# Kernel optimization log

Measured on AMD Instinct MI355X. Metric: run time of the kernel, lower is better.

Reference implementation:

```python
import jax, jax.numpy as jnp
import numpy as np

N_NODES = 50000
N_EDGES = 800000
N_GRAPHS = 128
IN_F = 768
NHID = 64
HID2 = NHID * 2  # 128
N_CLS = 2


def setup_inputs() -> dict:
    key = jax.random.key(0)
    ks = jax.random.split(key, 16)
    s = lambda k, shp, fan: jax.random.normal(k, shp, jnp.float32) / np.sqrt(fan)
    return {
        "x": jax.random.normal(ks[0], (N_NODES, IN_F), jnp.float32),
        "edge_index": jax.random.randint(ks[1], (2, N_EDGES), 0, N_NODES, jnp.int64),
        "batch": jnp.sort(jax.random.randint(ks[2], (N_NODES,), 0, N_GRAPHS, jnp.int64)),
        "W1": s(ks[3], (IN_F, HID2), IN_F),
        "as1": s(ks[4], (HID2,), HID2),
        "ad1": s(ks[5], (HID2,), HID2),
        "b1": jnp.zeros((HID2,), jnp.float32),
        "W2": s(ks[6], (HID2, HID2), HID2),
        "as2": s(ks[7], (HID2,), HID2),
        "ad2": s(ks[8], (HID2,), HID2),
        "b2": jnp.zeros((HID2,), jnp.float32),
        "fc1_w": s(ks[9], (HID2, NHID), HID2),
        "fc1_b": jnp.zeros((NHID,), jnp.float32),
        "fc2_w": s(ks[10], (NHID, N_CLS), NHID),
        "fc2_b": jnp.zeros((N_CLS,), jnp.float32),
    }


def _gat_conv(x, W, a_src, a_dst, b, src, dst):
    # PyG GATConv, heads=1, self-loops already included in (src, dst).
    xw = x @ W                                   # [N, F_out]
    e_src = xw @ a_src                           # [N]
    e_dst = xw @ a_dst                           # [N]
    e = jax.nn.leaky_relu(e_src[src] + e_dst[dst], 0.2)   # [E]
    m = jax.ops.segment_max(e, dst, num_segments=N_NODES)  # per-dst max (stable softmax)
    num = jnp.exp(e - m[dst])
    den = jax.ops.segment_sum(num, dst, num_segments=N_NODES)
    alpha = num / den[dst]                       # [E]
    out = jax.ops.segment_sum(alpha[:, None] * xw[src], dst, num_segments=N_NODES)
    return out + b


def reference(x, edge_index, batch, W1, as1, ad1, b1, W2, as2, ad2, b2,
              fc1_w, fc1_b, fc2_w, fc2_b):
    # add self loops (PyG GATConv default add_self_loops=True)
    loops = jnp.arange(N_NODES, dtype=edge_index.dtype)
    src = jnp.concatenate([edge_index[0], loops])
    dst = jnp.concatenate([edge_index[1], loops])

    h = jax.nn.selu(_gat_conv(x, W1, as1, ad1, b1, src, dst))
    h = jax.nn.selu(_gat_conv(h, W2, as2, ad2, b2, src, dst))

    # global mean pool over graphs
    sums = jax.ops.segment_sum(h, batch, num_segments=N_GRAPHS)          # [G, HID2]
    cnts = jax.ops.segment_sum(jnp.ones((N_NODES,), h.dtype), batch, num_segments=N_GRAPHS)
    pooled = jax.nn.selu(sums / jnp.maximum(cnts, 1.0)[:, None])

    g = jax.nn.selu(pooled @ fc1_w + fc1_b)      # dropout is identity in eval mode
    logits = g @ fc2_w + fc2_b
    return jax.nn.log_softmax(logits, axis=-1)
```

## Files before the change

kernel.cpp:

```cpp
#include <hip/hip_runtime.h>
#include <math.h>

#define N_NODES  50000
#define N_EDGES  800000
#define E_TOT    (N_EDGES + N_NODES)
#define N_GRAPHS 128
#define IN_F     768
#define HID2     128
#define NHID     64

typedef __attribute__((ext_vector_type(8))) short bf16x8;
typedef __attribute__((ext_vector_type(4))) float f32x4;
typedef __attribute__((ext_vector_type(4))) unsigned short us4;

__device__ __forceinline__ float selu_f(float x) {
    const float alpha = 1.6732632423543772f;
    const float scale = 1.0507009873554805f;
    return scale * (x > 0.f ? x : alpha * (expf(x) - 1.f));
}

__device__ __forceinline__ unsigned short f2bf(float f) {
    unsigned u = __float_as_uint(f);
    u += 0x7FFFu + ((u >> 16) & 1u);
    return (unsigned short)(u >> 16);
}
__device__ __forceinline__ float bflo(unsigned q) { return __uint_as_float(q << 16); }
__device__ __forceinline__ float bfhi(unsigned q) { return __uint_as_float(q & 0xffff0000u); }

__global__ void setup_k(const float* __restrict__ W1, const float* __restrict__ W2,
                        unsigned short* __restrict__ Wt1, unsigned short* __restrict__ Wt2,
                        unsigned* __restrict__ deg,
                        float* __restrict__ es1, float* __restrict__ ed1,
                        float* __restrict__ es2, float* __restrict__ ed2) {
    int i = blockIdx.x * blockDim.x + threadIdx.x;
    if (i < N_NODES) {
        deg[i] = 0u;
        es1[i] = 0.f; ed1[i] = 0.f;
        es2[i] = 0.f; ed2[i] = 0.f;
    }
    if (i < 128 * IN_F) {
        int n = i / IN_F, k = i - n * IN_F;
        Wt1[i] = f2bf(W1[(long)k * 128 + n]);
    }
    if (i < 128 * HID2) {
        int n = i >> 7, k = i & 127;
        Wt2[i] = f2bf(W2[(long)k * 128 + n]);
    }
}

#define LDA2 72
template<bool ABF16, bool OUTBF16>
__global__ __launch_bounds__(256) void gemm_mfma(
        const void* __restrict__ Av, const unsigned short* __restrict__ Bt,
        void* __restrict__ Cv, int M, int K,
        const float* __restrict__ a_s, const float* __restrict__ a_d,
        float* __restrict__ es, float* __restrict__ ed) {
    __shared__ unsigned short As[64 * LDA2];
    __shared__ unsigned short Bs[128 * LDA2];
    const float* Af = (const float*)Av;
    const unsigned short* Ab = (const unsigned short*)Av;
    const int tid  = threadIdx.x;
    const int row0 = blockIdx.x * 64;
    const int w    = tid >> 6;
    const int lane = tid & 63;
    const int quad = lane >> 4;
    const int l16  = lane & 15;
    const int m_off = (w & 1) * 32;
    const int n_off = (w >> 1) * 64;

    f32x4 acc[2][4];
#pragma unroll
    for (int mi = 0; mi < 2; mi++)
#pragma unroll
        for (int ni = 0; ni < 4; ni++)
            acc[mi][ni] = (f32x4){0.f, 0.f, 0.f, 0.f};

    float4 aR[4];
    bf16x8 aRb[2];
    bf16x8 bR[4];
    if (ABF16) {
#pragma unroll
        for (int i = 0; i < 2; i++) {
            int p = tid + i * 256;
            int r = p >> 3, c8 = p & 7;
            int gr = row0 + r;
            aRb[i] = (gr < M) ? *(const bf16x8*)&Ab[(long)gr * K + c8 * 8]
                              : (bf16x8){0,0,0,0,0,0,0,0};
        }
    } else {
#pragma unroll
        for (int i = 0; i < 4; i++) {
            int p = tid + i * 256;
            int r = p >> 4, c4 = p & 15;
            int gr = row0 + r;
            aR[i] = (gr < M) ? *(const float4*)&Af[(long)gr * K + c4 * 4]
                             : make_float4(0.f, 0.f, 0.f, 0.f);
        }
    }
#pragma unroll
    for (int i = 0; i < 4; i++) {
        int c = tid + i * 256;
        int n = c >> 3, koff = (c & 7) * 8;
        bR[i] = *(const bf16x8*)&Bt[(long)n * K + koff];
    }

    for (int k0 = 0; k0 < K; k0 += 64) {
        if (ABF16) {
#pragma unroll
            for (int i = 0; i < 2; i++) {
                int p = tid + i * 256;
                int r = p >> 3, c8 = p & 7;
                *(bf16x8*)&As[r * LDA2 + c8 * 8] = aRb[i];
            }
        } else {
#pragma unroll
            for (int i = 0; i < 4; i++) {
                int p = tid + i * 256;
                int r = p >> 4, c4 = p & 15;
                us4 o;
                o.x = f2bf(aR[i].x); o.y = f2bf(aR[i].y);
                o.z = f2bf(aR[i].z); o.w = f2bf(aR[i].w);
                *(us4*)&As[r * LDA2 + c4 * 4] = o;
            }
        }
#pragma unroll
        for (int i = 0; i < 4; i++) {
            int c = tid + i * 256;
            int n = c >> 3, koff = (c & 7) * 8;
            *(bf16x8*)&Bs[n * LDA2 + koff] = bR[i];
        }
        __syncthreads();

        if (k0 + 64 < K) {
            int k1 = k0 + 64;
            if (ABF16) {
#pragma unroll
                for (int i = 0; i < 2; i++) {
                    int p = tid + i * 256;
                    int r = p >> 3, c8 = p & 7;
                    int gr = row0 + r;
                    aRb[i] = (gr < M) ? *(const bf16x8*)&Ab[(long)gr * K + k1 + c8 * 8]
                                      : (bf16x8){0,0,0,0,0,0,0,0};
                }
            } else {
#pragma unroll
                for (int i = 0; i < 4; i++) {
                    int p = tid + i * 256;
                    int r = p >> 4, c4 = p & 15;
                    int gr = row0 + r;
                    aR[i] = (gr < M) ? *(const float4*)&Af[(long)gr * K + k1 + c4 * 4]
                                     : make_float4(0.f, 0.f, 0.f, 0.f);
                }
            }
#pragma unroll
            for (int i = 0; i < 4; i++) {
                int c = tid + i * 256;
                int n = c >> 3, koff = (c & 7) * 8;
                bR[i] = *(const bf16x8*)&Bt[(long)n * K + k1 + koff];
            }
        }

        bf16x8 af[2][2], bfr[2][4];
#pragma unroll
        for (int kk = 0; kk < 2; kk++) {
#pragma unroll
            for (int mi = 0; mi < 2; mi++)
                af[kk][mi] = *(const bf16x8*)&As[(m_off + mi * 16 + l16) * LDA2 + kk * 32 + quad * 8];
#pragma unroll
            for (int ni = 0; ni < 4; ni++)
                bfr[kk][ni] = *(const bf16x8*)&Bs[(n_off + ni * 16 + l16) * LDA2 + kk * 32 + quad * 8];
        }
#pragma unroll
        for (int kk = 0; kk < 2; kk++)
#pragma unroll
            for (int mi = 0; mi < 2; mi++)
#pragma unroll
                for (int ni = 0; ni < 4; ni++)
                    acc[mi][ni] = __builtin_amdgcn_mfma_f32_16x16x32_bf16(
                        af[kk][mi], bfr[kk][ni], acc[mi][ni], 0, 0, 0);
        __syncthreads();
    }

    float as_v[4], ad_v[4];
#pragma unroll
    for (int ni = 0; ni < 4; ni++) {
        int col = n_off + ni * 16 + l16;
        as_v[ni] = a_s[col];
        ad_v[ni] = a_d[col];
    }

#pragma unroll
    for (int mi = 0; mi < 2; mi++)
#pragma unroll
        for (int r = 0; r < 4; r++) {
            int row = row0 + m_off + mi * 16 + quad * 4 + r;
            float ps = 0.f, pd = 0.f;
#pragma unroll
            for (int ni = 0; ni < 4; ni++) {
                float v = acc[mi][ni][r];
                ps = fmaf(v, as_v[ni], ps);
                pd = fmaf(v, ad_v[ni], pd);
            }
#pragma unroll
            for (int o = 1; o < 16; o <<= 1) {
                ps += __shfl_xor(ps, o);
                pd += __shfl_xor(pd, o);
            }
            if (row < M) {
                if (l16 == 0) {
                    atomicAdd(es + row, ps);
                    atomicAdd(ed + row, pd);
                }
                if (OUTBF16) {
                    unsigned short* C16 = (unsigned short*)Cv;
#pragma unroll
                    for (int ni = 0; ni < 4; ni++)
                        C16[(long)row * 128 + n_off + ni * 16 + l16] = f2bf(acc[mi][ni][r]);
                } else {
                    float* Cf = (float*)Cv;
#pragma unroll
                    for (int ni = 0; ni < 4; ni++)
                        Cf[(long)row * 128 + n_off + ni * 16 + l16] = acc[mi][ni][r];
                }
            }
        }
}

__global__ void deg_hist(const int* __restrict__ ei, unsigned* __restrict__ deg) {
    int e = blockIdx.x * blockDim.x + threadIdx.x;
    if (e < N_EDGES) atomicAdd(&deg[ei[N_EDGES + e]], 1u);
}

__global__ __launch_bounds__(256) void scan_seed(const unsigned* __restrict__ deg,
                                                 unsigned* __restrict__ row_ptr,
                                                 unsigned* __restrict__ cursor,
                                                 unsigned* __restrict__ csr_src) {
    __shared__ unsigned psum_s[4];
    __shared__ unsigned wsum[4];
    int tid = threadIdx.x;
    int wid = tid >> 6, lane = tid & 63;
    int chunk0 = blockIdx.x * 256;

    unsigned psum = 0;
    for (int i = tid; i < chunk0; i += 256) psum += deg[i] + 1u;
    for (int o = 32; o; o >>= 1) psum += __shfl_xor(psum, o);
    if (lane == 0) psum_s[wid] = psum;

    int i = chunk0 + tid;
    unsigned v = (i < N_NODES) ? deg[i] + 1u : 0u;
    unsigned x = v;
    for (int o = 1; o < 64; o <<= 1) {
        unsigned y = __shfl_up(x, o);
        if (lane >= o) x += y;
    }
    if (lane == 63) wsum[wid] = x;
    __syncthreads();
    unsigned base = psum_s[0] + psum_s[1] + psum_s[2] + psum_s[3];
    unsigned wbase = 0;
    for (int k = 0; k < wid; k++) wbase += wsum[k];
    if (i < N_NODES) {
        unsigned rp = base + wbase + x - v;
        row_ptr[i] = rp;
        csr_src[rp] = (unsigned)i;
        cursor[i] = rp + 1;
        if (i == N_NODES - 1) row_ptr[N_NODES] = rp + v;
    }
}

__global__ void csr_scatter(const int* __restrict__ ei,
                            unsigned* __restrict__ cursor, unsigned* __restrict__ csr_src) {
    int e = blockIdx.x * blockDim.x + threadIdx.x;
    if (e >= N_EDGES) return;
    int d = ei[N_EDGES + e];
    unsigned p = atomicAdd(&cursor[d], 1u);
    csr_src[p] = (unsigned)ei[e];
}

template<bool OUTBF16>
__global__ __launch_bounds__(256) void gat_agg(
        const unsigned* __restrict__ row_ptr, const unsigned* __restrict__ csr_src,
        const float* __restrict__ e_src, const float* __restrict__ e_dst,
        const unsigned short* __restrict__ xw, const float* __restrict__ bias,
        void* __restrict__ outv) {
    __shared__ float2 buf[4][64];
    int wv = threadIdx.x >> 6;
    int node = blockIdx.x * 4 + wv;
    if (node >= N_NODES) return;
    int lane = threadIdx.x & 63;
    int half = lane >> 5;
    int fl   = lane & 31;
    unsigned beg = row_ptr[node], end = row_ptr[node + 1];
    int deg = (int)(end - beg);
    float ed = e_dst[node];
    const unsigned short* xwf = xw + fl * 4;

    float ax = 0.f, ay = 0.f, az = 0.f, aw = 0.f, den = 0.f;
    for (int base = 0; base < deg; base += 64) {
        int i = base + lane;
        float num = 0.f;
        unsigned s = 0u;
        if (i < deg) {
            s = csr_src[beg + i];
            float e = e_src[s] + ed;
            e = e > 0.f ? e : 0.2f * e;
            num = __expf(e);
            den += num;
        }
        float2 pk; pk.x = num; pk.y = __uint_as_float(s);
        buf[wv][lane] = pk;

        int cnt = deg - base; if (cnt > 64) cnt = 64;
        int steps = (cnt + 1) >> 1;
        int t = 0;
        for (; t + 4 <= steps; t += 4) {
            float2 p0 = buf[wv][2 * (t + 0) + half];
            float2 p1 = buf[wv][2 * (t + 1) + half];
            float2 p2 = buf[wv][2 * (t + 2) + half];
            float2 p3 = buf[wv][2 * (t + 3) + half];
            uint2 q0 = *(const uint2*)&xwf[(long)__float_as_uint(p0.y) * HID2];
            uint2 q1 = *(const uint2*)&xwf[(long)__float_as_uint(p1.y) * HID2];
            uint2 q2 = *(const uint2*)&xwf[(long)__float_as_uint(p2.y) * HID2];
            uint2 q3 = *(const uint2*)&xwf[(long)__float_as_uint(p3.y) * HID2];
            ax = fmaf(p0.x, bflo(q0.x), ax); ay = fmaf(p0.x, bfhi(q0.x), ay);
            az = fmaf(p0.x, bflo(q0.y), az); aw = fmaf(p0.x, bfhi(q0.y), aw);
            ax = fmaf(p1.x, bflo(q1.x), ax); ay = fmaf(p1.x, bfhi(q1.x), ay);
            az = fmaf(p1.x, bflo(q1.y), az); aw = fmaf(p1.x, bfhi(q1.y), aw);
            ax = fmaf(p2.x, bflo(q2.x), ax); ay = fmaf(p2.x, bfhi(q2.x), ay);
            az = fmaf(p2.x, bflo(q2.y), az); aw = fmaf(p2.x, bfhi(q2.y), aw);
            ax = fmaf(p3.x, bflo(q3.x), ax); ay = fmaf(p3.x, bfhi(q3.x), ay);
            az = fmaf(p3.x, bflo(q3.y), az); aw = fmaf(p3.x, bfhi(q3.y), aw);
        }
        for (; t < steps; t++) {
            float2 p = buf[wv][2 * t + half];
            uint2 q = *(const uint2*)&xwf[(long)__float_as_uint(p.y) * HID2];
            ax = fmaf(p.x, bflo(q.x), ax); ay = fmaf(p.x, bfhi(q.x), ay);
            az = fmaf(p.x, bflo(q.y), az); aw = fmaf(p.x, bfhi(q.y), aw);
        }
    }
    ax += __shfl_xor(ax, 32); ay += __shfl_xor(ay, 32);
    az += __shfl_xor(az, 32); aw += __shfl_xor(aw, 32);
    for (int o = 32; o; o >>= 1) den += __shfl_xor(den, o);
    float inv = 1.f / den;
    float v0 = selu_f(fmaf(ax, inv, bias[fl * 4 + 0]));
    float v1 = selu_f(fmaf(ay, inv, bias[fl * 4 + 1]));
    float v2 = selu_f(fmaf(az, inv, bias[fl * 4 + 2]));
    float v3 = selu_f(fmaf(aw, inv, bias[fl * 4 + 3]));
    if (half == 0) {
        if (OUTBF16) {
            uint2 o;
            o.x = ((unsigned)f2bf(v1) << 16) | (unsigned)f2bf(v0);
            o.y = ((unsigned)f2bf(v3) << 16) | (unsigned)f2bf(v2);
            *(uint2*)((unsigned short*)outv + (long)node * HID2 + fl * 4) = o;
        } else {
            float4 o = make_float4(v0, v1, v2, v3);
            *(float4*)((float*)outv + (long)node * HID2 + fl * 4) = o;
        }
    }
}

__global__ __launch_bounds__(256) void pool_head(
        const float* __restrict__ h, const int* __restrict__ batch,
        const float* __restrict__ fc1w, const float* __restrict__ fc1b,
        const float* __restrict__ fc2w, const float* __restrict__ fc2b,
        float* __restrict__ out) {
    __shared__ float pooled_s[HID2];
    __shared__ float part[HID2];
    __shared__ float g_s[NHID];
    int g = blockIdx.x;
    int lo = 0, hi = N_NODES;
    while (lo < hi) { int mid = (lo + hi) >> 1; if (batch[mid] < g) lo = mid + 1; else hi = mid; }
    int start = lo;
    hi = N_NODES;
    while (lo < hi) { int mid = (lo + hi) >> 1; if (batch[mid] < g + 1) lo = mid + 1; else hi = mid; }
    int end = lo;

    int f = threadIdx.x & 127, half = threadIdx.x >> 7;
    float acc = 0.f;
    for (int n = start + half; n < end; n += 2) acc += h[(long)n * HID2 + f];
    if (half == 0) part[f] = acc;
    __syncthreads();
    if (half == 1) {
        float c = (float)(end - start);
        c = c > 1.f ? c : 1.f;
        pooled_s[f] = selu_f((part[f] + acc) / c);
    }
    __syncthreads();
    int j = threadIdx.x;
    if (j < NHID) {
        float a = fc1b[j];
#pragma unroll
        for (int k = 0; k < HID2; k++) a = fmaf(pooled_s[k], fc1w[k * NHID + j], a);
        g_s[j] = selu_f(a);
    }
    __syncthreads();
    if (j == 0) {
        float l0 = fc2b[0], l1 = fc2b[1];
#pragma unroll
        for (int k = 0; k < NHID; k++) {
            float v = g_s[k];
            l0 = fmaf(v, fc2w[2 * k + 0], l0);
            l1 = fmaf(v, fc2w[2 * k + 1], l1);
        }
        float m = fmaxf(l0, l1);
        float lse = m + logf(expf(l0 - m) + expf(l1 - m));
        out[g * 2 + 0] = l0 - lse;
        out[g * 2 + 1] = l1 - lse;
    }
}

extern "C" void kernel_launch(void* const* d_in, const int* in_sizes, int n_in,
                              void* d_out, int out_size, void* d_ws, size_t ws_size,
                              hipStream_t stream) {
    const float* x     = (const float*)d_in[0];
    const int*   ei    = (const int*)d_in[1];
    const int*   batch = (const int*)d_in[2];
    const float* W1    = (const float*)d_in[3];
    const float* as1   = (const float*)d_in[4];
    const float* ad1   = (const float*)d_in[5];
    const float* b1    = (const float*)d_in[6];
    const float* W2    = (const float*)d_in[7];
    const float* as2   = (const float*)d_in[8];
    const float* ad2   = (const float*)d_in[9];
    const float* b2    = (const float*)d_in[10];
    const float* fc1w  = (const float*)d_in[11];
    const float* fc1b  = (const float*)d_in[12];
    const float* fc2w  = (const float*)d_in[13];
    const float* fc2b  = (const float*)d_in[14];
    float* out = (float*)d_out;

    const long NH = (long)N_NODES * HID2;
    unsigned short* xwb = (unsigned short*)d_ws;
    unsigned short* h1b = xwb + NH;
    float*    B2      = (float*)(h1b + NH);
    float*    es1     = B2 + NH;
    float*    ed1     = es1 + N_NODES;
    float*    es2     = ed1 + N_NODES;
    float*    ed2     = es2 + N_NODES;
    unsigned* deg     = (unsigned*)(ed2 + N_NODES);
    unsigned* cursor  = deg + N_NODES;
    unsigned* row_ptr = cursor + N_NODES;
    unsigned* csr_src = row_ptr + N_NODES + 1;
    unsigned short* Wt1 = (unsigned short*)(csr_src + E_TOT);
    unsigned short* Wt2 = Wt1 + 128 * IN_F;

    const int TB = 256;
    const int gNode = (N_NODES + TB - 1) / TB;
    const int gEdge = (N_EDGES + TB - 1) / TB;
    const int gGemm = (N_NODES + 63) / 64;
    const int gAgg  = (N_NODES + 3) / 4;

    setup_k<<<(128 * IN_F + TB - 1) / TB, TB, 0, stream>>>(W1, W2, Wt1, Wt2, deg,
                                                           es1, ed1, es2, ed2);
    deg_hist<<<gEdge, TB, 0, stream>>>(ei, deg);
    scan_seed<<<gNode, TB, 0, stream>>>(deg, row_ptr, cursor, csr_src);
    csr_scatter<<<gEdge, TB, 0, stream>>>(ei, cursor, csr_src);

    gemm_mfma<false, true><<<gGemm, 256, 0, stream>>>(x, Wt1, xwb, N_NODES, IN_F,
                                                      as1, ad1, es1, ed1);
    gat_agg<true><<<gAgg, 256, 0, stream>>>(row_ptr, csr_src, es1, ed1, xwb, b1, h1b);

    gemm_mfma<true, true><<<gGemm, 256, 0, stream>>>(h1b, Wt2, xwb, N_NODES, HID2,
                                                     as2, ad2, es2, ed2);
    gat_agg<false><<<gAgg, 256, 0, stream>>>(row_ptr, csr_src, es2, ed2, xwb, b2, B2);

    pool_head<<<N_GRAPHS, 256, 0, stream>>>(B2, batch, fc1w, fc1b, fc2w, fc2b, out);
}
```

Measured before the change: 529.0 us.

## Split GAT aggregation into alpha pass and XCD-partitioned feature-slice gather

GEMM output is now written in a column-slab layout: four slabs of 32 bf16 features, each stored contiguously per node. Attention softmax weights are computed once per edge by a separate alpha kernel into a buffer. A gather kernel then maps each of four feature slabs to a pair of XCDs, chosen from the block id, so that each XCD's L2 only caches a quarter of the feature table. This trades an extra kernel and extra alpha writes and reads for better cache locality in the random gather, and it relies on the assumption that blocks are dispatched round-robin across XCDs.

```diff
diff --git a/kernel.cpp b/kernel.cpp
--- a/kernel.cpp
+++ b/kernel.cpp
@@ -49,10 +49,10 @@
 }
 
 #define LDA2 72
-template<bool ABF16, bool OUTBF16>
+template<bool ABF16>
 __global__ __launch_bounds__(256) void gemm_mfma(
         const void* __restrict__ Av, const unsigned short* __restrict__ Bt,
-        void* __restrict__ Cv, int M, int K,
+        unsigned short* __restrict__ Cq, int M, int K,
         const float* __restrict__ a_s, const float* __restrict__ a_d,
         float* __restrict__ es, float* __restrict__ ed) {
     __shared__ unsigned short As[64 * LDA2];
@@ -211,16 +211,11 @@
                     atomicAdd(es + row, ps);
                     atomicAdd(ed + row, pd);
                 }
-                if (OUTBF16) {
-                    unsigned short* C16 = (unsigned short*)Cv;
-#pragma unroll
-                    for (int ni = 0; ni < 4; ni++)
-                        C16[(long)row * 128 + n_off + ni * 16 + l16] = f2bf(acc[mi][ni][r]);
-                } else {
-                    float* Cf = (float*)Cv;
-#pragma unroll
-                    for (int ni = 0; ni < 4; ni++)
-                        Cf[(long)row * 128 + n_off + ni * 16 + l16] = acc[mi][ni][r];
+#pragma unroll
+                for (int ni = 0; ni < 4; ni++) {
+                    int col = n_off + ni * 16 + l16;
+                    Cq[((long)(col >> 5) * N_NODES + row) * 32 + (col & 31)] =
+                        f2bf(acc[mi][ni][r]);
                 }
             }
         }
@@ -276,85 +271,110 @@
     csr_src[p] = (unsigned)ei[e];
 }
 
-template<bool OUTBF16>
-__global__ __launch_bounds__(256) void gat_agg(
+__global__ __launch_bounds__(256) void gat_alpha(
         const unsigned* __restrict__ row_ptr, const unsigned* __restrict__ csr_src,
         const float* __restrict__ e_src, const float* __restrict__ e_dst,
-        const unsigned short* __restrict__ xw, const float* __restrict__ bias,
-        void* __restrict__ outv) {
-    __shared__ float2 buf[4][64];
-    int wv = threadIdx.x >> 6;
-    int node = blockIdx.x * 4 + wv;
+        float* __restrict__ alpha) {
+    int hw = threadIdx.x >> 5;
+    int node = blockIdx.x * 8 + hw;
     if (node >= N_NODES) return;
-    int lane = threadIdx.x & 63;
-    int half = lane >> 5;
-    int fl   = lane & 31;
+    int l = threadIdx.x & 31;
     unsigned beg = row_ptr[node], end = row_ptr[node + 1];
     int deg = (int)(end - beg);
     float ed = e_dst[node];
-    const unsigned short* xwf = xw + fl * 4;
-
-    float ax = 0.f, ay = 0.f, az = 0.f, aw = 0.f, den = 0.f;
-    for (int base = 0; base < deg; base += 64) {
-        int i = base + lane;
+    float den = 0.f;
+
+    if (deg <= 32) {
         float num = 0.f;
-        unsigned s = 0u;
-        if (i < deg) {
-            s = csr_src[beg + i];
+        if (l < deg) {
+            unsigned s = csr_src[beg + l];
             float e = e_src[s] + ed;
             e = e > 0.f ? e : 0.2f * e;
             num = __expf(e);
-            den += num;
-        }
-        float2 pk; pk.x = num; pk.y = __uint_as_float(s);
-        buf[wv][lane] = pk;
-
-        int cnt = deg - base; if (cnt > 64) cnt = 64;
-        int steps = (cnt + 1) >> 1;
-        int t = 0;
-        for (; t + 4 <= steps; t += 4) {
-            float2 p0 = buf[wv][2 * (t + 0) + half];
-            float2 p1 = buf[wv][2 * (t + 1) + half];
-            float2 p2 = buf[wv][2 * (t + 2) + half];
-            float2 p3 = buf[wv][2 * (t + 3) + half];
-            uint2 q0 = *(const uint2*)&xwf[(long)__float_as_uint(p0.y) * HID2];
-            uint2 q1 = *(const uint2*)&xwf[(long)__float_as_uint(p1.y) * HID2];
-            uint2 q2 = *(const uint2*)&xwf[(long)__float_as_uint(p2.y) * HID2];
-            uint2 q3 = *(const uint2*)&xwf[(long)__float_as_uint(p3.y) * HID2];
-            ax = fmaf(p0.x, bflo(q0.x), ax); ay = fmaf(p0.x, bfhi(q0.x), ay);
-            az = fmaf(p0.x, bflo(q0.y), az); aw = fmaf(p0.x, bfhi(q0.y), aw);
-            ax = fmaf(p1.x, bflo(q1.x), ax); ay = fmaf(p1.x, bfhi(q1.x), ay);
-            az = fmaf(p1.x, bflo(q1.y), az); aw = fmaf(p1.x, bfhi(q1.y), aw);
-            ax = fmaf(p2.x, bflo(q2.x), ax); ay = fmaf(p2.x, bfhi(q2.x), ay);
-            az = fmaf(p2.x, bflo(q2.y), az); aw = fmaf(p2.x, bfhi(q2.y), aw);
-            ax = fmaf(p3.x, bflo(q3.x), ax); ay = fmaf(p3.x, bfhi(q3.x), ay);
-            az = fmaf(p3.x, bflo(q3.y), az); aw = fmaf(p3.x, bfhi(q3.y), aw);
-        }
-        for (; t < steps; t++) {
-            float2 p = buf[wv][2 * t + half];
-            uint2 q = *(const uint2*)&xwf[(long)__float_as_uint(p.y) * HID2];
-            ax = fmaf(p.x, bflo(q.x), ax); ay = fmaf(p.x, bfhi(q.x), ay);
-            az = fmaf(p.x, bflo(q.y), az); aw = fmaf(p.x, bfhi(q.y), aw);
-        }
-    }
-    ax += __shfl_xor(ax, 32); ay += __shfl_xor(ay, 32);
-    az += __shfl_xor(az, 32); aw += __shfl_xor(aw, 32);
-    for (int o = 32; o; o >>= 1) den += __shfl_xor(den, o);
-    float inv = 1.f / den;
-    float v0 = selu_f(fmaf(ax, inv, bias[fl * 4 + 0]));
-    float v1 = selu_f(fmaf(ay, inv, bias[fl * 4 + 1]));
-    float v2 = selu_f(fmaf(az, inv, bias[fl * 4 + 2]));
-    float v3 = selu_f(fmaf(aw, inv, bias[fl * 4 + 3]));
-    if (half == 0) {
-        if (OUTBF16) {
-            uint2 o;
-            o.x = ((unsigned)f2bf(v1) << 16) | (unsigned)f2bf(v0);
-            o.y = ((unsigned)f2bf(v3) << 16) | (unsigned)f2bf(v2);
-            *(uint2*)((unsigned short*)outv + (long)node * HID2 + fl * 4) = o;
-        } else {
-            float4 o = make_float4(v0, v1, v2, v3);
-            *(float4*)((float*)outv + (long)node * HID2 + fl * 4) = o;
-        }
+            den = num;
+        }
+        for (int o = 16; o; o >>= 1) den += __shfl_xor(den, o);
+        float inv = 1.f / den;
+        if (l < deg) alpha[beg + l] = num * inv;
+    } else {
+        for (int base = 0; base < deg; base += 32) {
+            int i = base + l;
+            if (i < deg) {
+                unsigned s = csr_src[beg + i];
+                float e = e_src[s] + ed;
+                e = e > 0.f ? e : 0.2f * e;
+                float num = __expf(e);
+                den += num;
+                alpha[beg + i] = num;
+            }
+        }
+        for (int o = 16; o; o >>= 1) den += __shfl_xor(den, o);
+        float inv = 1.f / den;
+        for (int i = l; i < deg; i += 32) alpha[beg + i] *= inv;
+    }
+}
+
+template<bool OUTBF16>
+__global__ __launch_bounds__(256) void gat_gather(
+        const unsigned* __restrict__ row_ptr, const unsigned* __restrict__ csr_src,
+        const float* __restrict__ alpha, const unsigned* __restrict__ xwq,
+        const float* __restrict__ bias, void* __restrict__ outv) {
+    int bid = blockIdx.x;
+    int xcd = bid & 7;
+    int q   = xcd >> 1;
+    int idx = (bid >> 3) * 2 + (xcd & 1);
+    if (idx * 16 >= N_NODES) return;
+    int g = threadIdx.x >> 4;
+    int node = idx * 16 + g;
+    if (node >= N_NODES) return;
+    int l = threadIdx.x & 15;
+    unsigned beg = row_ptr[node];
+    int deg = (int)(row_ptr[node + 1] - beg);
+    const unsigned* tbl = xwq + (long)q * N_NODES * 16 + l;
+
+    float a0 = 0.f, a1 = 0.f;
+    int t = 0;
+    for (; t + 8 <= deg; t += 8) {
+        unsigned s0 = csr_src[beg + t + 0]; float w0 = alpha[beg + t + 0];
+        unsigned s1 = csr_src[beg + t + 1]; float w1 = alpha[beg + t + 1];
+        unsigned s2 = csr_src[beg + t + 2]; float w2 = alpha[beg + t + 2];
+        unsigned s3 = csr_src[beg + t + 3]; float w3 = alpha[beg + t + 3];
+        unsigned s4 = csr_src[beg + t + 4]; float w4 = alpha[beg + t + 4];
+        unsigned s5 = csr_src[beg + t + 5]; float w5 = alpha[beg + t + 5];
+        unsigned s6 = csr_src[beg + t + 6]; float w6 = alpha[beg + t + 6];
+        unsigned s7 = csr_src[beg + t + 7]; float w7 = alpha[beg + t + 7];
+        unsigned u0 = tbl[(long)s0 * 16];
+        unsigned u1 = tbl[(long)s1 * 16];
+        unsigned u2 = tbl[(long)s2 * 16];
+        unsigned u3 = tbl[(long)s3 * 16];
+        unsigned u4 = tbl[(long)s4 * 16];
+        unsigned u5 = tbl[(long)s5 * 16];
+        unsigned u6 = tbl[(long)s6 * 16];
+        unsigned u7 = tbl[(long)s7 * 16];
+        a0 = fmaf(w0, bflo(u0), a0); a1 = fmaf(w0, bfhi(u0), a1);
+        a0 = fmaf(w1, bflo(u1), a0); a1 = fmaf(w1, bfhi(u1), a1);
+        a0 = fmaf(w2, bflo(u2), a0); a1 = fmaf(w2, bfhi(u2), a1);
+        a0 = fmaf(w3, bflo(u3), a0); a1 = fmaf(w3, bfhi(u3), a1);
+        a0 = fmaf(w4, bflo(u4), a0); a1 = fmaf(w4, bfhi(u4), a1);
+        a0 = fmaf(w5, bflo(u5), a0); a1 = fmaf(w5, bfhi(u5), a1);
+        a0 = fmaf(w6, bflo(u6), a0); a1 = fmaf(w6, bfhi(u6), a1);
+        a0 = fmaf(w7, bflo(u7), a0); a1 = fmaf(w7, bfhi(u7), a1);
+    }
+    for (; t < deg; t++) {
+        unsigned s = csr_src[beg + t]; float w = alpha[beg + t];
+        unsigned u = tbl[(long)s * 16];
+        a0 = fmaf(w, bflo(u), a0); a1 = fmaf(w, bfhi(u), a1);
+    }
+
+    float2 b = *(const float2*)&bias[q * 32 + l * 2];
+    float v0 = selu_f(a0 + b.x);
+    float v1 = selu_f(a1 + b.y);
+    if (OUTBF16) {
+        unsigned o = ((unsigned)f2bf(v1) << 16) | (unsigned)f2bf(v0);
+        *((unsigned*)outv + (long)node * 64 + q * 16 + l) = o;
+    } else {
+        float2 o = make_float2(v0, v1);
+        *(float2*)((float*)outv + (long)node * HID2 + q * 32 + l * 2) = o;
     }
 }
 
@@ -442,12 +462,14 @@
     unsigned* csr_src = row_ptr + N_NODES + 1;
     unsigned short* Wt1 = (unsigned short*)(csr_src + E_TOT);
     unsigned short* Wt2 = Wt1 + 128 * IN_F;
+    float*    alphaB  = (float*)(Wt2 + 128 * HID2);
 
     const int TB = 256;
     const int gNode = (N_NODES + TB - 1) / TB;
     const int gEdge = (N_EDGES + TB - 1) / TB;
     const int gGemm = (N_NODES + 63) / 64;
-    const int gAgg  = (N_NODES + 3) / 4;
+    const int gAlpha = (N_NODES + 7) / 8;
+    const int gGather = 12504;
 
     setup_k<<<(128 * IN_F + TB - 1) / TB, TB, 0, stream>>>(W1, W2, Wt1, Wt2, deg,
                                                            es1, ed1, es2, ed2);
@@ -455,13 +477,17 @@
     scan_seed<<<gNode, TB, 0, stream>>>(deg, row_ptr, cursor, csr_src);
     csr_scatter<<<gEdge, TB, 0, stream>>>(ei, cursor, csr_src);
 
-    gemm_mfma<false, true><<<gGemm, 256, 0, stream>>>(x, Wt1, xwb, N_NODES, IN_F,
-                                                      as1, ad1, es1, ed1);
-    gat_agg<true><<<gAgg, 256, 0, stream>>>(row_ptr, csr_src, es1, ed1, xwb, b1, h1b);
-
-    gemm_mfma<true, true><<<gGemm, 256, 0, stream>>>(h1b, Wt2, xwb, N_NODES, HID2,
-                                                     as2, ad2, es2, ed2);
-    gat_agg<false><<<gAgg, 256, 0, stream>>>(row_ptr, csr_src, es2, ed2, xwb, b2, B2);
+    gemm_mfma<false><<<gGemm, 256, 0, stream>>>(x, Wt1, xwb, N_NODES, IN_F,
+                                                as1, ad1, es1, ed1);
+    gat_alpha<<<gAlpha, TB, 0, stream>>>(row_ptr, csr_src, es1, ed1, alphaB);
+    gat_gather<true><<<gGather, TB, 0, stream>>>(row_ptr, csr_src, alphaB,
+                                                 (const unsigned*)xwb, b1, h1b);
+
+    gemm_mfma<true><<<gGemm, 256, 0, stream>>>(h1b, Wt2, xwb, N_NODES, HID2,
+                                               as2, ad2, es2, ed2);
+    gat_alpha<<<gAlpha, TB, 0, stream>>>(row_ptr, csr_src, es2, ed2, alphaB);
+    gat_gather<false><<<gGather, TB, 0, stream>>>(row_ptr, csr_src, alphaB,
+                                                  (const unsigned*)xwb, b2, B2);
 
     pool_head<<<N_GRAPHS, 256, 0, stream>>>(B2, batch, fc1w, fc1b, fc2w, fc2b, out);
 }
```

Result: slower. 569.4 us (+7.6%).
